# Performance work log

Hardware: AMD Instinct MI355X
Metric: run time of the kernel (lower is better)

The kernel has to match this reference:

```python
import jax, jax.numpy as jnp
import numpy as np

N_IN = 1024
N_OUT = 2048
EMBED_DIM = 1024  # == n_in so multi-layer path type-checks
LAYERS = 2
T, B = 128, 64


def setup_inputs() -> dict:
    key = jax.random.key(0)
    ks = jax.random.split(key, 8)
    s_in = 1.0 / np.sqrt(N_IN)
    s_out = 1.0 / np.sqrt(N_OUT)
    return {
        "xt": jax.random.normal(ks[0], (T, B, N_IN), jnp.float32),
        "ct_forward": jnp.zeros((LAYERS, B, N_OUT), jnp.float32),
        # weights stored [in, out] (transposed vs torch Linear)
        "Wx": jax.random.uniform(ks[1], (N_IN, N_OUT), jnp.float32, -s_in, s_in),
        "Wf": jax.random.uniform(ks[2], (N_IN, N_OUT), jnp.float32, -s_in, s_in),
        "bf": jnp.zeros((N_OUT,), jnp.float32),
        "Wr": jax.random.uniform(ks[3], (N_IN, N_OUT), jnp.float32, -s_in, s_in),
        "br": jnp.zeros((N_OUT,), jnp.float32),
        "Wcx": jax.random.uniform(ks[4], (N_IN, N_OUT), jnp.float32, -s_in, s_in),
        "bcx": jnp.zeros((N_OUT,), jnp.float32),
        "Wcl": jax.random.uniform(ks[5], (N_OUT, EMBED_DIM), jnp.float32, -s_out, s_out),
        "bcl": jnp.zeros((EMBED_DIM,), jnp.float32),
    }


def _one_layer(x, c0, Wx, Wf, bf, Wr, br, Wcx, bcx):
    # x: [T, B, n_in]; c0: [B, n_out]
    # batch all projections over time (compute-dense GEMMs)
    xp = jnp.einsum("tbi,io->tbo", x, Wx)                     # x_t projection
    f = jax.nn.sigmoid(jnp.einsum("tbi,io->tbo", x, Wf) + bf)  # forget gate
    r = jax.nn.sigmoid(jnp.einsum("tbi,io->tbo", x, Wr) + br)  # reset gate
    cx = jnp.einsum("tbi,io->tbo", x, Wcx) + bcx               # highway path

    def step(c, inp):
        f_t, xp_t = inp
        c_new = f_t * c + (1.0 - f_t) * xp_t
        return c_new, c_new

    c_last, c_seq = jax.lax.scan(step, c0, (f, xp))
    h = r * jnp.tanh(c_seq) + (1.0 - r) * cx
    return h, c_last


def reference(xt, ct_forward, Wx, Wf, bf, Wr, br, Wcx, bcx, Wcl, bcl):
    x = xt
    c_last = ct_forward[0]
    for l in range(LAYERS):
        if x.shape[2] == N_OUT:  # layers >= 2: project back to embed_dim (= n_in)
            x = jnp.einsum("tbo,oe->tbe", x, Wcl) + bcl
        x, c_last = _one_layer(x, ct_forward[l], Wx, Wf, bf, Wr, br, Wcx, bcx)
    # dropout p=0.0 -> identity
    return x, c_last
```

## Files before the change

kernel.cpp:

```cpp
#include <hip/hip_runtime.h>

#define TT 128
#define BB 64
#define NIN 1024
#define NOUT 2048
#define MR (TT*BB)

typedef unsigned short u16;
typedef __attribute__((ext_vector_type(8))) __bf16 bf16x8;
typedef __attribute__((ext_vector_type(4))) float f32x4;
typedef __attribute__((ext_vector_type(8))) unsigned short u16x8;

static __device__ __forceinline__ u16 f2bf(float f) {
    union { float f; unsigned u; } v; v.f = f;
    unsigned r = v.u + 0x7fffu + ((v.u >> 16) & 1u);
    return (u16)(r >> 16);
}
static __device__ __forceinline__ float bf2f(u16 x) {
    union { unsigned u; float f; } v; v.u = ((unsigned)x) << 16;
    return v.f;
}

__global__ void k_cvt_chunk(const float* __restrict__ s, u16* __restrict__ d, int M_, int K_) {
    __shared__ float t[64][33];
    int m0 = blockIdx.x * 64, k0 = blockIdx.y * 32;
    int ml = threadIdx.x >> 3, kl = (threadIdx.x & 7) * 4;
    #pragma unroll
    for (int p = 0; p < 2; ++p) {
        float4 v = *(const float4*)&s[(size_t)(m0 + ml + p * 32) * K_ + k0 + kl];
        t[ml + p * 32][kl] = v.x; t[ml + p * 32][kl + 1] = v.y;
        t[ml + p * 32][kl + 2] = v.z; t[ml + p * 32][kl + 3] = v.w;
    }
    __syncthreads();
    int q = threadIdx.x >> 6, row = threadIdx.x & 63;
    u16x8 o;
    #pragma unroll
    for (int j = 0; j < 8; ++j) o[j] = f2bf(t[row][q * 8 + j]);
    *(u16x8*)&d[(((size_t)(k0 >> 3) + q) * M_ + m0 + row) * 8] = o;
}

__global__ void k_wT_chunk(const float* __restrict__ s, u16* __restrict__ d,
                           int K_, int N_, int OUTM, int row_off) {
    __shared__ float t[32][65];
    int k0 = blockIdx.y * 32, n0 = blockIdx.x * 64;
    int kl = threadIdx.x >> 6, nl = threadIdx.x & 63;
    #pragma unroll
    for (int p = 0; p < 8; ++p)
        t[kl + p * 4][nl] = s[(size_t)(k0 + kl + p * 4) * N_ + n0 + nl];
    __syncthreads();
    int q = threadIdx.x >> 6, row = threadIdx.x & 63;
    u16x8 o;
    #pragma unroll
    for (int j = 0; j < 8; ++j) o[j] = f2bf(t[q * 8 + j][row]);
    *(u16x8*)&d[(((size_t)(k0 >> 3) + q) * OUTM + row_off + n0 + row) * 8] = o;
}

__global__ void k_bias_pack(const float* __restrict__ bf_, const float* __restrict__ br_,
                            const float* __restrict__ bcx_, float* __restrict__ ball) {
    int i = blockIdx.x * 256 + threadIdx.x;
    int g = i >> 11, n = i & 2047;
    float v = 0.f;
    if (g == 1) v = bf_[n];
    else if (g == 2) v = br_[n];
    else if (g == 3) v = bcx_[n];
    ball[i] = v;
}

#define GLL16(SRC, DST) __builtin_amdgcn_global_load_lds( \
    (const __attribute__((address_space(1))) void*)(SRC), \
    (__attribute__((address_space(3))) void*)(DST), 16, 0, 0)
#define SBAR() __builtin_amdgcn_s_barrier()
#define SCHED0() __builtin_amdgcn_sched_barrier(0)
#define VM8 asm volatile("s_waitcnt vmcnt(8)" ::: "memory")
#define VM4 asm volatile("s_waitcnt vmcnt(4)" ::: "memory")
#define VM0 asm volatile("s_waitcnt vmcnt(0)" ::: "memory")

__global__ __launch_bounds__(512, 2) void k_gemm8(
    const u16* __restrict__ A, const u16* __restrict__ BT,
    const float* __restrict__ bias, u16* __restrict__ outG,
    int M, int NB, int K)
{
    __shared__ __align__(16) u16 L[65536];

    const int tid = threadIdx.x;
    const int w = tid >> 6, lane = tid & 63;
    const int wr = w >> 2, wc = w & 3;
    const int lr = lane & 15, kq = lane >> 4;
    const int flat = blockIdx.y * gridDim.x + blockIdx.x;
    const int xcd = flat & 7, bi = flat >> 3;
    const int n0 = (xcd * 4 + (bi & 3)) * 256;
    const int m0 = (bi >> 2) * 256;
    const int nk = K >> 6;

    const int t1 = tid + 512;
    const u16* aS0 = A + ((size_t)(tid >> 8) * M + m0 + (tid & 255)) * 8;
    const u16* aS1 = A + ((size_t)(t1 >> 8) * M + m0 + (t1 & 255)) * 8;
    const u16* bS0 = BT + ((size_t)(tid >> 8) * NB + n0 + (tid & 255)) * 8;
    const u16* bS1 = BT + ((size_t)(t1 >> 8) * NB + n0 + (t1 & 255)) * 8;
    const int aD0 = (w * 64) * 8, aD1 = (w * 64 + 512) * 8;

    f32x4 acc[8][4] = {};

#define STAGE(TAU, KH, BUFB) { \
    const size_t oA = ((size_t)(TAU) * 8 + (KH) * 4) * (size_t)M * 8; \
    const size_t oB = ((size_t)(TAU) * 8 + (KH) * 4) * (size_t)NB * 8; \
    GLL16(aS0 + oA, &L[(BUFB) + (KH) * 8192 + aD0]); \
    GLL16(aS1 + oA, &L[(BUFB) + (KH) * 8192 + aD1]); \
    GLL16(bS0 + oB, &L[(BUFB) + 16384 + (KH) * 8192 + aD0]); \
    GLL16(bS1 + oB, &L[(BUFB) + 16384 + (KH) * 8192 + aD1]); }

#define LDA(BUFB, KH, RB) { _Pragma("unroll") for (int i = 0; i < 4; ++i) \
    aF[i] = *(const bf16x8*)&L[(BUFB) + (KH) * 8192 + (kq * 256 + wr * 128 + (RB) * 64 + i * 16 + lr) * 8]; }
#define LDB(BUFB, KH) { _Pragma("unroll") for (int j = 0; j < 4; ++j) \
    bF[j] = *(const bf16x8*)&L[(BUFB) + 16384 + (KH) * 8192 + (kq * 256 + wc * 64 + j * 16 + lr) * 8]; }
#define MM(RO) { __builtin_amdgcn_s_setprio(1); \
    _Pragma("unroll") for (int i = 0; i < 4; ++i) \
        _Pragma("unroll") for (int j = 0; j < 4; ++j) \
            acc[(RO) + i][j] = __builtin_amdgcn_mfma_f32_16x16x32_bf16(aF[i], bF[j], acc[(RO) + i][j], 0, 0, 0); \
    __builtin_amdgcn_s_setprio(0); }

    STAGE(0, 0, 0); STAGE(0, 1, 0); STAGE(1, 0, 32768);
    VM8; SBAR(); SCHED0();

    for (int it = 0; it < nk / 2; ++it) {
        const int t = 2 * it;
        const bool st2 = (t + 2) < nk, st3 = (t + 3) < nk;
        bf16x8 aF[4], bF[4];
        LDA(0, 0, 0); LDB(0, 0); STAGE(t + 1, 1, 32768);
        SBAR(); MM(0); SBAR();
        LDA(0, 0, 1);
        SBAR(); MM(4); VM8; SBAR(); SCHED0();
        LDA(0, 1, 0); LDB(0, 1); if (st2) STAGE(t + 2, 0, 0);
        SBAR(); MM(0); SBAR();
        LDA(0, 1, 1);
        SBAR(); MM(4); if (st2) { VM8; } else { VM4; } SBAR(); SCHED0();
        LDA(32768, 0, 0); LDB(32768, 0); if (st2) STAGE(t + 2, 1, 0);
        SBAR(); MM(0); SBAR();
        LDA(32768, 0, 1);
        SBAR(); MM(4); if (st2) { VM8; } else { VM0; } SBAR(); SCHED0();
        LDA(32768, 1, 0); LDB(32768, 1); if (st3) STAGE(t + 3, 0, 32768);
        SBAR(); MM(0); SBAR();
        LDA(32768, 1, 1);
        SBAR(); MM(4);
        if (st2) { if (st3) { VM8; } else { VM4; } } else { VM0; }
        SBAR(); SCHED0();
    }
#undef STAGE
#undef LDA
#undef LDB
#undef MM

    const size_t GM2 = (size_t)M << 11;
    #pragma unroll
    for (int i = 0; i < 8; ++i) {
        int r0 = m0 + wr * 128 + i * 16 + kq * 4;
        #pragma unroll
        for (int j = 0; j < 4; ++j) {
            int gc = n0 + wc * 64 + j * 16 + lr;
            float bv = bias[gc];
            int g = gc >> 11;
            bool sig = (g == 1 || g == 2);
            size_t base = (size_t)g * GM2 + (size_t)(gc & 2047);
            #pragma unroll
            for (int q = 0; q < 4; ++q) {
                float v = acc[i][j][q] + bv;
                if (sig) v = 1.f / (1.f + __expf(-v));
                outG[base + (size_t)(r0 + q) * 2048] = f2bf(v);
            }
        }
    }
}

__global__ __launch_bounds__(512, 2) void k_gemm4(
    const u16* __restrict__ A, const u16* __restrict__ BT,
    const float* __restrict__ bias, u16* __restrict__ outC,
    int M, int NB, int K)
{
    constexpr int BM = 128;
    constexpr int BUF = BM * 32 + 8192;
    __shared__ __align__(16) u16 L[4 * BUF];

    const int tid = threadIdx.x;
    const int w = tid >> 6, lane = tid & 63;
    const int wr = w >> 2, wc = w & 3;
    const int lr = lane & 15, kq = lane >> 4;
    const int gx = gridDim.x;
    const int nwg = gx * gridDim.y;
    const int flat = blockIdx.y * gx + blockIdx.x;
    const int swz = (flat & 7) * (nwg >> 3) + (flat >> 3);
    const int m0 = (swz / gx) * BM, n0 = (swz % gx) * 256;
    const int nk = K >> 5;

    const u16* aSrc1; int aDst1;
    {
        int q = tid >> 7, row = tid & 127;
        aSrc1 = A + ((size_t)q * M + m0 + row) * 8;
        aDst1 = (w * 64) * 8;
    }
    const u16* bSrc[2]; int bDst[2];
    #pragma unroll
    for (int l = 0; l < 2; ++l) {
        int tc = tid + l * 512;
        bSrc[l] = BT + ((size_t)(tc >> 8) * NB + n0 + (tc & 255)) * 8;
        bDst[l] = BM * 32 + (w * 64 + l * 512) * 8;
    }
    const size_t aStep = (size_t)32 * M;
    const size_t bStep = (size_t)32 * NB;
    const int rdA = wr * 64 + lr;
    const int rdB = wc * 64 + lr;

    f32x4 acc[4][4] = {};
    bf16x8 aP0[4], bP0[4], aP1[4], bP1[4];

    #pragma unroll
    for (int p = 0; p < 3; ++p) {
        GLL16(aSrc1 + (size_t)p * aStep, &L[p * BUF + aDst1]);
        #pragma unroll
        for (int l = 0; l < 2; ++l) GLL16(bSrc[l] + (size_t)p * bStep, &L[p * BUF + bDst[l]]);
    }
    asm volatile("s_waitcnt vmcnt(3)" ::: "memory");
    SBAR(); SCHED0();
    #pragma unroll
    for (int i = 0; i < 4; ++i) aP0[i] = *(const bf16x8*)&L[(kq * BM + rdA + i * 16) * 8];
    #pragma unroll
    for (int j = 0; j < 4; ++j) bP0[j] = *(const bf16x8*)&L[BM * 32 + (kq * 256 + rdB + j * 16) * 8];

#define ITER4(KT, CUR, NXT) { \
    const int kt_ = (KT); \
    const int tn = (kt_ + 1 < nk) ? kt_ + 1 : nk - 1; \
    const int nb = (tn & 3) * BUF; \
    if (kt_ + 3 < nk) { \
        const size_t sa = (size_t)(kt_ + 3) * aStep, sb_ = (size_t)(kt_ + 3) * bStep; \
        const int wb = ((kt_ + 3) & 3) * BUF; \
        GLL16(aSrc1 + sa, &L[wb + aDst1]); \
        _Pragma("unroll") for (int l = 0; l < 2; ++l) GLL16(bSrc[l] + sb_, &L[wb + bDst[l]]); \
    } \
    __builtin_amdgcn_s_setprio(1); \
    _Pragma("unroll") for (int i = 0; i < 4; ++i) \
        _Pragma("unroll") for (int j = 0; j < 4; ++j) \
            acc[i][j] = __builtin_amdgcn_mfma_f32_16x16x32_bf16(aP##CUR[i], bP##CUR[j], acc[i][j], 0, 0, 0); \
    _Pragma("unroll") for (int i = 0; i < 4; ++i) \
        aP##NXT[i] = *(const bf16x8*)&L[nb + (kq * BM + rdA + i * 16) * 8]; \
    _Pragma("unroll") for (int j = 0; j < 4; ++j) \
        bP##NXT[j] = *(const bf16x8*)&L[nb + BM * 32 + (kq * 256 + rdB + j * 16) * 8]; \
    __builtin_amdgcn_s_setprio(0); \
    asm volatile("s_waitcnt vmcnt(3)" ::: "memory"); \
    SBAR(); SCHED0(); }

    for (int kt4 = 0; kt4 < nk; kt4 += 4) {
        ITER4(kt4 + 0, 0, 1);
        ITER4(kt4 + 1, 1, 0);
        ITER4(kt4 + 2, 0, 1);
        ITER4(kt4 + 3, 1, 0);
    }
#undef ITER4

    #pragma unroll
    for (int i = 0; i < 4; ++i) {
        int r0 = m0 + wr * 64 + i * 16 + kq * 4;
        #pragma unroll
        for (int j = 0; j < 4; ++j) {
            int gc = n0 + wc * 64 + j * 16 + lr;
            float bv = bias[gc];
            size_t base = ((size_t)(gc >> 3) * M) * 8 + (size_t)(gc & 7);
            #pragma unroll
            for (int q = 0; q < 4; ++q)
                outC[base + (size_t)(r0 + q) * 8] = f2bf(acc[i][j][q] + bv);
        }
    }
}

__global__ void k_scan(const u16* __restrict__ G, const float* __restrict__ c0,
                       u16* __restrict__ hb, float* __restrict__ hf,
                       float* __restrict__ cout)
{
    int idx = blockIdx.x * 256 + threadIdx.x;
    int b = idx >> 11, n = idx & 2047;
    float c = c0[idx];
    const size_t GM = (size_t)MR * 2048;
    const size_t hcBase = ((size_t)(n >> 3) * MR) * 8 + (size_t)(n & 7);
    for (int t = 0; t < TT; ++t) {
        int m = t * BB + b;
        size_t p = ((size_t)m << 11) + (size_t)n;
        float xp = bf2f(G[p]);
        float f  = bf2f(G[GM + p]);
        float r  = bf2f(G[2 * GM + p]);
        float cx = bf2f(G[3 * GM + p]);
        c = f * c + (1.f - f) * xp;
        float h = r * tanhf(c) + (1.f - r) * cx;
        if (hb) hb[hcBase + (size_t)m * 8] = f2bf(h);
        if (hf) hf[p] = h;
    }
    if (cout) cout[idx] = c;
}

extern "C" void kernel_launch(void* const* d_in, const int* in_sizes, int n_in,
                              void* d_out, int out_size, void* d_ws, size_t ws_size,
                              hipStream_t stream)
{
    const float* xt  = (const float*)d_in[0];
    const float* ctf = (const float*)d_in[1];
    const float* Wx  = (const float*)d_in[2];
    const float* Wf  = (const float*)d_in[3];
    const float* bfp = (const float*)d_in[4];
    const float* Wr  = (const float*)d_in[5];
    const float* brp = (const float*)d_in[6];
    const float* Wcx = (const float*)d_in[7];
    const float* bcx = (const float*)d_in[8];
    const float* Wcl = (const float*)d_in[9];
    const float* bcl = (const float*)d_in[10];
    float* out = (float*)d_out;

    char* ws = (char*)d_ws;
    u16* x0 = (u16*)ws;       ws += (size_t)MR * NIN * 2;
    u16* x2 = (u16*)ws;       ws += (size_t)MR * NIN * 2;
    u16* h1 = (u16*)ws;       ws += (size_t)MR * NOUT * 2;
    u16* WTall = (u16*)ws;    ws += (size_t)4 * NOUT * NIN * 2;
    u16* WclT = (u16*)ws;     ws += (size_t)NIN * NOUT * 2;
    float* ball = (float*)ws; ws += (size_t)4 * NOUT * 4;
    u16* G = (u16*)ws;        ws += (size_t)4 * MR * NOUT * 2;

    k_cvt_chunk<<<dim3(MR / 64, NIN / 32), 256, 0, stream>>>(xt, x0, MR, NIN);
    k_wT_chunk<<<dim3(NOUT / 64, NIN / 32), 256, 0, stream>>>(Wx,  WTall, NIN, NOUT, 4 * NOUT, 0 * NOUT);
    k_wT_chunk<<<dim3(NOUT / 64, NIN / 32), 256, 0, stream>>>(Wf,  WTall, NIN, NOUT, 4 * NOUT, 1 * NOUT);
    k_wT_chunk<<<dim3(NOUT / 64, NIN / 32), 256, 0, stream>>>(Wr,  WTall, NIN, NOUT, 4 * NOUT, 2 * NOUT);
    k_wT_chunk<<<dim3(NOUT / 64, NIN / 32), 256, 0, stream>>>(Wcx, WTall, NIN, NOUT, 4 * NOUT, 3 * NOUT);
    k_wT_chunk<<<dim3(NIN / 64, NOUT / 32), 256, 0, stream>>>(Wcl, WclT, NOUT, NIN, NIN, 0);
    k_bias_pack<<<32, 256, 0, stream>>>(bfp, brp, bcx, ball);

    k_gemm8<<<dim3(32, 32), 512, 0, stream>>>(x0, WTall, ball, G, MR, 4 * NOUT, NIN);
    k_scan<<<(BB * NOUT) / 256, 256, 0, stream>>>(G, ctf, h1, (float*)nullptr, (float*)nullptr);

    k_gemm4<<<dim3(NIN / 256, MR / 128), 512, 0, stream>>>(h1, WclT, bcl, x2, MR, NIN, NOUT);

    k_gemm8<<<dim3(32, 32), 512, 0, stream>>>(x2, WTall, ball, G, MR, 4 * NOUT, NIN);
    k_scan<<<(BB * NOUT) / 256, 256, 0, stream>>>(G, ctf + (size_t)BB * NOUT, (u16*)nullptr, out, out + (size_t)MR * NOUT);
}
```

Measured before the change: 486.3 us.

## Restructure 256x256 GEMM mainloop into 4-stage K32 pipeline with register prefetch

The big GEMM kernel's mainloop moves from a double-buffered 64-wide K step with split halves to a 4-deep ring of 32-wide K stages. Each stage prefetches three tiles ahead and also preloads the next tile's A and B fragments into registers while the second half of the MFMAs runs. The goal is to hide LDS read latency and global load latency behind compute and to cut barrier stalls. The second GEMM's tail wait now drains to zero when no further loads are issued, which fixes a possible read of data that has not arrived yet. The new pipeline keeps more fragment registers live and runs more barriers per unit of K.

After: 503.9 us. +3.6%, slower.

```diff
diff --git a/kernel.cpp b/kernel.cpp
--- a/kernel.cpp
+++ b/kernel.cpp
@@ -73,6 +73,7 @@
 #define SCHED0() __builtin_amdgcn_sched_barrier(0)
 #define VM8 asm volatile("s_waitcnt vmcnt(8)" ::: "memory")
 #define VM4 asm volatile("s_waitcnt vmcnt(4)" ::: "memory")
+#define VM3 asm volatile("s_waitcnt vmcnt(3)" ::: "memory")
 #define VM0 asm volatile("s_waitcnt vmcnt(0)" ::: "memory")
 
 __global__ __launch_bounds__(512, 2) void k_gemm8(
@@ -80,7 +81,8 @@
     const float* __restrict__ bias, u16* __restrict__ outG,
     int M, int NB, int K)
 {
-    __shared__ __align__(16) u16 L[65536];
+    constexpr int BUF = 16384;
+    __shared__ __align__(16) u16 L[4 * BUF];
 
     const int tid = threadIdx.x;
     const int w = tid >> 6, lane = tid & 63;
@@ -90,65 +92,74 @@
     const int xcd = flat & 7, bi = flat >> 3;
     const int n0 = (xcd * 4 + (bi & 3)) * 256;
     const int m0 = (bi >> 2) * 256;
-    const int nk = K >> 6;
+    const int nk = K >> 5;
 
     const int t1 = tid + 512;
     const u16* aS0 = A + ((size_t)(tid >> 8) * M + m0 + (tid & 255)) * 8;
     const u16* aS1 = A + ((size_t)(t1 >> 8) * M + m0 + (t1 & 255)) * 8;
     const u16* bS0 = BT + ((size_t)(tid >> 8) * NB + n0 + (tid & 255)) * 8;
     const u16* bS1 = BT + ((size_t)(t1 >> 8) * NB + n0 + (t1 & 255)) * 8;
-    const int aD0 = (w * 64) * 8, aD1 = (w * 64 + 512) * 8;
+    const int aD0 = (w * 64) * 8, aD1 = (512 + w * 64) * 8;
+    const int bD0 = 8192 + aD0, bD1 = 8192 + aD1;
+    const size_t aStep = (size_t)32 * M, bStep = (size_t)32 * NB;
+
+    const int rA0 = (kq * 256 + wr * 128 + lr) * 8;
+    const int rA1 = (kq * 256 + wr * 128 + 64 + lr) * 8;
+    const int rB  = (kq * 256 + wc * 64 + lr) * 8;
 
     f32x4 acc[8][4] = {};
-
-#define STAGE(TAU, KH, BUFB) { \
-    const size_t oA = ((size_t)(TAU) * 8 + (KH) * 4) * (size_t)M * 8; \
-    const size_t oB = ((size_t)(TAU) * 8 + (KH) * 4) * (size_t)NB * 8; \
-    GLL16(aS0 + oA, &L[(BUFB) + (KH) * 8192 + aD0]); \
-    GLL16(aS1 + oA, &L[(BUFB) + (KH) * 8192 + aD1]); \
-    GLL16(bS0 + oB, &L[(BUFB) + 16384 + (KH) * 8192 + aD0]); \
-    GLL16(bS1 + oB, &L[(BUFB) + 16384 + (KH) * 8192 + aD1]); }
-
-#define LDA(BUFB, KH, RB) { _Pragma("unroll") for (int i = 0; i < 4; ++i) \
-    aF[i] = *(const bf16x8*)&L[(BUFB) + (KH) * 8192 + (kq * 256 + wr * 128 + (RB) * 64 + i * 16 + lr) * 8]; }
-#define LDB(BUFB, KH) { _Pragma("unroll") for (int j = 0; j < 4; ++j) \
-    bF[j] = *(const bf16x8*)&L[(BUFB) + 16384 + (KH) * 8192 + (kq * 256 + wc * 64 + j * 16 + lr) * 8]; }
-#define MM(RO) { __builtin_amdgcn_s_setprio(1); \
-    _Pragma("unroll") for (int i = 0; i < 4; ++i) \
-        _Pragma("unroll") for (int j = 0; j < 4; ++j) \
-            acc[(RO) + i][j] = __builtin_amdgcn_mfma_f32_16x16x32_bf16(aF[i], bF[j], acc[(RO) + i][j], 0, 0, 0); \
-    __builtin_amdgcn_s_setprio(0); }
-
-    STAGE(0, 0, 0); STAGE(0, 1, 0); STAGE(1, 0, 32768);
-    VM8; SBAR(); SCHED0();
-
-    for (int it = 0; it < nk / 2; ++it) {
-        const int t = 2 * it;
-        const bool st2 = (t + 2) < nk, st3 = (t + 3) < nk;
-        bf16x8 aF[4], bF[4];
-        LDA(0, 0, 0); LDB(0, 0); STAGE(t + 1, 1, 32768);
-        SBAR(); MM(0); SBAR();
-        LDA(0, 0, 1);
-        SBAR(); MM(4); VM8; SBAR(); SCHED0();
-        LDA(0, 1, 0); LDB(0, 1); if (st2) STAGE(t + 2, 0, 0);
-        SBAR(); MM(0); SBAR();
-        LDA(0, 1, 1);
-        SBAR(); MM(4); if (st2) { VM8; } else { VM4; } SBAR(); SCHED0();
-        LDA(32768, 0, 0); LDB(32768, 0); if (st2) STAGE(t + 2, 1, 0);
-        SBAR(); MM(0); SBAR();
-        LDA(32768, 0, 1);
-        SBAR(); MM(4); if (st2) { VM8; } else { VM0; } SBAR(); SCHED0();
-        LDA(32768, 1, 0); LDB(32768, 1); if (st3) STAGE(t + 3, 0, 32768);
-        SBAR(); MM(0); SBAR();
-        LDA(32768, 1, 1);
-        SBAR(); MM(4);
-        if (st2) { if (st3) { VM8; } else { VM4; } } else { VM0; }
-        SBAR(); SCHED0();
-    }
+    bf16x8 aF0[4], aF1[4], bF0[4], bF1[4];
+
+#define STAGE(TAU) { const size_t _oA = (size_t)(TAU) * aStep, _oB = (size_t)(TAU) * bStep; \
+    const int _wb = ((TAU) & 3) * BUF; \
+    GLL16(aS0 + _oA, &L[_wb + aD0]); GLL16(aS1 + _oA, &L[_wb + aD1]); \
+    GLL16(bS0 + _oB, &L[_wb + bD0]); GLL16(bS1 + _oB, &L[_wb + bD1]); }
+#define LDAP(DST, BB_) { _Pragma("unroll") for (int i = 0; i < 4; ++i) \
+    DST[i] = *(const bf16x8*)&L[(BB_) + rA0 + i * 128]; }
+#define LDAG(DST, BB_) { _Pragma("unroll") for (int i = 0; i < 4; ++i) \
+    DST[i] = *(const bf16x8*)&L[(BB_) + rA1 + i * 128]; }
+#define LDBP(DST, BB_) { _Pragma("unroll") for (int j = 0; j < 4; ++j) \
+    DST[j] = *(const bf16x8*)&L[(BB_) + 8192 + rB + j * 128]; }
+#define MM0(BF) { _Pragma("unroll") for (int i = 0; i < 4; ++i) \
+    _Pragma("unroll") for (int j = 0; j < 4; ++j) \
+        acc[i][j] = __builtin_amdgcn_mfma_f32_16x16x32_bf16(aF0[i], BF[j], acc[i][j], 0, 0, 0); }
+#define MM4(BF) { _Pragma("unroll") for (int i = 0; i < 4; ++i) \
+    _Pragma("unroll") for (int j = 0; j < 4; ++j) \
+        acc[i + 4][j] = __builtin_amdgcn_mfma_f32_16x16x32_bf16(aF1[i], BF[j], acc[i + 4][j], 0, 0, 0); }
+
+#define ITER(T_, BC, BN_) { \
+    const int t_ = (T_); \
+    const bool st3 = (t_ + 3) < nk, st2 = (t_ + 2) < nk; \
+    const int tn = (t_ + 1 < nk) ? t_ + 1 : nk - 1; \
+    const int cb = (t_ & 3) * BUF, nb = (tn & 3) * BUF; \
+     \
+    if (st3) STAGE(t_ + 3); \
+    LDAG(aF1, cb); \
+    if (st3) { VM8; } else if (st2) { VM4; } else { VM0; } \
+    SBAR(); \
+    __builtin_amdgcn_s_setprio(1); MM0(bF##BC); __builtin_amdgcn_s_setprio(0); \
+    SBAR(); \
+     \
+    LDAP(aF0, nb); LDBP(bF##BN_, nb); \
+    SBAR(); \
+    __builtin_amdgcn_s_setprio(1); MM4(bF##BC); __builtin_amdgcn_s_setprio(0); \
+    SBAR(); SCHED0(); }
+
+    STAGE(0); STAGE(1); STAGE(2);
+    VM8; SBAR();
+    LDAP(aF0, 0); LDBP(bF0, 0);
+
+    for (int t2 = 0; t2 < nk; t2 += 2) {
+        ITER(t2 + 0, 0, 1);
+        ITER(t2 + 1, 1, 0);
+    }
+#undef ITER
 #undef STAGE
-#undef LDA
-#undef LDB
-#undef MM
+#undef LDAP
+#undef LDAG
+#undef LDBP
+#undef MM0
+#undef MM4
 
     const size_t GM2 = (size_t)M << 11;
     #pragma unroll
@@ -218,7 +229,7 @@
         #pragma unroll
         for (int l = 0; l < 2; ++l) GLL16(bSrc[l] + (size_t)p * bStep, &L[p * BUF + bDst[l]]);
     }
-    asm volatile("s_waitcnt vmcnt(3)" ::: "memory");
+    VM3;
     SBAR(); SCHED0();
     #pragma unroll
     for (int i = 0; i < 4; ++i) aP0[i] = *(const bf16x8*)&L[(kq * BM + rdA + i * 16) * 8];
@@ -244,7 +255,7 @@
     _Pragma("unroll") for (int j = 0; j < 4; ++j) \
         bP##NXT[j] = *(const bf16x8*)&L[nb + BM * 32 + (kq * 256 + rdB + j * 16) * 8]; \
     __builtin_amdgcn_s_setprio(0); \
-    asm volatile("s_waitcnt vmcnt(3)" ::: "memory"); \
+    if (kt_ + 3 < nk) { VM3; } else { VM0; } \
     SBAR(); SCHED0(); }
 
     for (int kt4 = 0; kt4 < nk; kt4 += 4) {
```

## Restructure GEMM main loop into finer-grained A/B staging with explicit LDS waits

Applied to the files above, without the earlier changes.

Reworks the k_gemm8 main loop so each 64-wide K tile is staged as separate A and B halves, interleaved with the four 16-MFMA sub-blocks. Each sub-block now consumes two K-slices per MFMA pair, with explicit lgkmcnt waits before the math. Loads for the next tile are spread across the sub-phases to overlap global-to-LDS traffic with MFMA work and cut register pressure from the fragments. The second GEMM's tail wait now drains to zero on the last iterations. This adds extra barriers and relies on the new LDS layout being consistent between writes and reads.

After: 479.2 us. About the same (-1.5%).

```diff
diff --git a/kernel.cpp b/kernel.cpp
--- a/kernel.cpp
+++ b/kernel.cpp
@@ -71,9 +71,8 @@
     (__attribute__((address_space(3))) void*)(DST), 16, 0, 0)
 #define SBAR() __builtin_amdgcn_s_barrier()
 #define SCHED0() __builtin_amdgcn_sched_barrier(0)
-#define VM8 asm volatile("s_waitcnt vmcnt(8)" ::: "memory")
-#define VM4 asm volatile("s_waitcnt vmcnt(4)" ::: "memory")
-#define VM0 asm volatile("s_waitcnt vmcnt(0)" ::: "memory")
+#define LGKM0 do { asm volatile("s_waitcnt lgkmcnt(0)" ::: "memory"); SCHED0(); } while (0)
+#define VMW(N) asm volatile("s_waitcnt vmcnt(" #N ")" ::: "memory")
 
 __global__ __launch_bounds__(512, 2) void k_gemm8(
     const u16* __restrict__ A, const u16* __restrict__ BT,
@@ -92,63 +91,89 @@
     const int m0 = (bi >> 2) * 256;
     const int nk = K >> 6;
 
-    const int t1 = tid + 512;
-    const u16* aS0 = A + ((size_t)(tid >> 8) * M + m0 + (tid & 255)) * 8;
-    const u16* aS1 = A + ((size_t)(t1 >> 8) * M + m0 + (t1 & 255)) * 8;
-    const u16* bS0 = BT + ((size_t)(tid >> 8) * NB + n0 + (tid & 255)) * 8;
-    const u16* bS1 = BT + ((size_t)(t1 >> 8) * NB + n0 + (t1 & 255)) * 8;
-    const int aD0 = (w * 64) * 8, aD1 = (w * 64 + 512) * 8;
+    const u16* aS = A + ((size_t)(tid >> 7) * M + m0 + (tid & 127)) * 8;
+    const u16* bS = BT + ((size_t)(tid >> 7) * NB + n0 + (tid & 127)) * 8;
+    const size_t aT = (size_t)64 * M, bT = (size_t)64 * NB;
+    const size_t aL = (size_t)32 * M, bL = (size_t)32 * NB;
+
+    const int rdA = wr * 8192 + (kq * 128 + lr) * 8;
+    const int rdB = 16384 + (wc >> 1) * 8192 + (kq * 128 + (wc & 1) * 64 + lr) * 8;
 
     f32x4 acc[8][4] = {};
-
-#define STAGE(TAU, KH, BUFB) { \
-    const size_t oA = ((size_t)(TAU) * 8 + (KH) * 4) * (size_t)M * 8; \
-    const size_t oB = ((size_t)(TAU) * 8 + (KH) * 4) * (size_t)NB * 8; \
-    GLL16(aS0 + oA, &L[(BUFB) + (KH) * 8192 + aD0]); \
-    GLL16(aS1 + oA, &L[(BUFB) + (KH) * 8192 + aD1]); \
-    GLL16(bS0 + oB, &L[(BUFB) + 16384 + (KH) * 8192 + aD0]); \
-    GLL16(bS1 + oB, &L[(BUFB) + 16384 + (KH) * 8192 + aD1]); }
-
-#define LDA(BUFB, KH, RB) { _Pragma("unroll") for (int i = 0; i < 4; ++i) \
-    aF[i] = *(const bf16x8*)&L[(BUFB) + (KH) * 8192 + (kq * 256 + wr * 128 + (RB) * 64 + i * 16 + lr) * 8]; }
-#define LDB(BUFB, KH) { _Pragma("unroll") for (int j = 0; j < 4; ++j) \
-    bF[j] = *(const bf16x8*)&L[(BUFB) + 16384 + (KH) * 8192 + (kq * 256 + wc * 64 + j * 16 + lr) * 8]; }
-#define MM(RO) { __builtin_amdgcn_s_setprio(1); \
+    bf16x8 aA[4][2], bLo[2][2], bHi[2][2];
+
+#define STAGEA(TAU, H) { const size_t _o = (size_t)(TAU) * aT + (H) * 1024; \
+    const int _d = (((TAU) & 1) << 15) + ((H) << 13) + w * 512; \
+    GLL16(aS + _o, &L[_d]); GLL16(aS + _o + aL, &L[_d + 4096]); }
+#define STAGEB(TAU, H) { const size_t _o = (size_t)(TAU) * bT + (H) * 1024; \
+    const int _d = (((TAU) & 1) << 15) + 16384 + ((H) << 13) + w * 512; \
+    GLL16(bS + _o, &L[_d]); GLL16(bS + _o + bL, &L[_d + 4096]); }
+#define LDA(S, H) { _Pragma("unroll") for (int i = 0; i < 4; ++i) \
+    _Pragma("unroll") for (int ks = 0; ks < 2; ++ks) \
+        aA[i][ks] = *(const bf16x8*)&L[(S) + rdA + ks * 4096 + ((H) * 64 + i * 16) * 8]; }
+#define LDB(DST, S, H) { _Pragma("unroll") for (int j = 0; j < 2; ++j) \
+    _Pragma("unroll") for (int ks = 0; ks < 2; ++ks) \
+        DST[j][ks] = *(const bf16x8*)&L[(S) + rdB + ks * 4096 + ((H) * 32 + j * 16) * 8]; }
+#define MM16(BSET, RO, CO) { __builtin_amdgcn_s_setprio(1); \
     _Pragma("unroll") for (int i = 0; i < 4; ++i) \
-        _Pragma("unroll") for (int j = 0; j < 4; ++j) \
-            acc[(RO) + i][j] = __builtin_amdgcn_mfma_f32_16x16x32_bf16(aF[i], bF[j], acc[(RO) + i][j], 0, 0, 0); \
+    _Pragma("unroll") for (int j = 0; j < 2; ++j) \
+    _Pragma("unroll") for (int ks = 0; ks < 2; ++ks) \
+        acc[(RO) + i][(CO) + j] = __builtin_amdgcn_mfma_f32_16x16x32_bf16( \
+            aA[i][ks], BSET[j][ks], acc[(RO) + i][(CO) + j], 0, 0, 0); \
     __builtin_amdgcn_s_setprio(0); }
 
-    STAGE(0, 0, 0); STAGE(0, 1, 0); STAGE(1, 0, 32768);
-    VM8; SBAR(); SCHED0();
+    STAGEB(0, 0); STAGEB(0, 1); STAGEA(0, 0); STAGEA(0, 1);
+    STAGEB(1, 0); STAGEB(1, 1);
+    VMW(4); SBAR(); SCHED0();
 
     for (int it = 0; it < nk / 2; ++it) {
         const int t = 2 * it;
-        const bool st2 = (t + 2) < nk, st3 = (t + 3) < nk;
-        bf16x8 aF[4], bF[4];
-        LDA(0, 0, 0); LDB(0, 0); STAGE(t + 1, 1, 32768);
-        SBAR(); MM(0); SBAR();
-        LDA(0, 0, 1);
-        SBAR(); MM(4); VM8; SBAR(); SCHED0();
-        LDA(0, 1, 0); LDB(0, 1); if (st2) STAGE(t + 2, 0, 0);
-        SBAR(); MM(0); SBAR();
-        LDA(0, 1, 1);
-        SBAR(); MM(4); if (st2) { VM8; } else { VM4; } SBAR(); SCHED0();
-        LDA(32768, 0, 0); LDB(32768, 0); if (st2) STAGE(t + 2, 1, 0);
-        SBAR(); MM(0); SBAR();
-        LDA(32768, 0, 1);
-        SBAR(); MM(4); if (st2) { VM8; } else { VM0; } SBAR(); SCHED0();
-        LDA(32768, 1, 0); LDB(32768, 1); if (st3) STAGE(t + 3, 0, 32768);
-        SBAR(); MM(0); SBAR();
-        LDA(32768, 1, 1);
-        SBAR(); MM(4);
-        if (st2) { if (st3) { VM8; } else { VM4; } } else { VM0; }
+        const int s = 0, s1 = 32768;
+        const bool st = (t + 2) < nk;
+        LDA(s, 0); LDB(bLo, s, 0);
+        STAGEA(t + 1, 0);
+        SBAR(); LGKM0;
+        MM16(bLo, 0, 0);
+        SBAR();
+        LDB(bHi, s, 1);
+        STAGEA(t + 1, 1);
+        SBAR(); LGKM0;
+        MM16(bHi, 0, 2);
+        SBAR();
+        LDA(s, 1);
+        if (st) STAGEB(t + 2, 0);
+        SBAR(); LGKM0;
+        MM16(bLo, 4, 0);
+        SBAR();
+        if (st) STAGEB(t + 2, 1);
+        MM16(bHi, 4, 2);
+        if (st) { VMW(4); } else { VMW(0); }
         SBAR(); SCHED0();
-    }
-#undef STAGE
+        LDA(s1, 0); LDB(bLo, s1, 0);
+        if (st) STAGEA(t + 2, 0);
+        SBAR(); LGKM0;
+        MM16(bLo, 0, 0);
+        SBAR();
+        LDB(bHi, s1, 1);
+        if (st) STAGEA(t + 2, 1);
+        SBAR(); LGKM0;
+        MM16(bHi, 0, 2);
+        SBAR();
+        LDA(s1, 1);
+        if (st) STAGEB(t + 3, 0);
+        SBAR(); LGKM0;
+        MM16(bLo, 4, 0);
+        SBAR();
+        if (st) STAGEB(t + 3, 1);
+        MM16(bHi, 4, 2);
+        if (st) { VMW(4); } else { VMW(0); }
+        SBAR(); SCHED0();
+    }
+#undef STAGEA
+#undef STAGEB
 #undef LDA
 #undef LDB
-#undef MM
+#undef MM16
 
     const size_t GM2 = (size_t)M << 11;
     #pragma unroll
@@ -218,7 +243,7 @@
         #pragma unroll
         for (int l = 0; l < 2; ++l) GLL16(bSrc[l] + (size_t)p * bStep, &L[p * BUF + bDst[l]]);
     }
-    asm volatile("s_waitcnt vmcnt(3)" ::: "memory");
+    VMW(3);
     SBAR(); SCHED0();
     #pragma unroll
     for (int i = 0; i < 4; ++i) aP0[i] = *(const bf16x8*)&L[(kq * BM + rdA + i * 16) * 8];
@@ -244,7 +269,7 @@
     _Pragma("unroll") for (int j = 0; j < 4; ++j) \
         bP##NXT[j] = *(const bf16x8*)&L[nb + BM * 32 + (kq * 256 + rdB + j * 16) * 8]; \
     __builtin_amdgcn_s_setprio(0); \
-    asm volatile("s_waitcnt vmcnt(3)" ::: "memory"); \
+    if (kt_ + 3 < nk) { VMW(3); } else { VMW(0); } \
     SBAR(); SCHED0(); }
 
     for (int kt4 = 0; kt4 < nk; kt4 += 4) {
```
